# Optimization experiments

Hardware: AMD Instinct MI355X
Metric: run time of the kernel (lower is better)

The kernel has to match this reference:

```python
import jax, jax.numpy as jnp
import numpy as np

N = 100000   # nodes
E = 1600000  # edges
FEAT = 128
HID = 128
TGT = 64
L = 3
G = 512      # graphs in batch


def setup_inputs() -> dict:
    key = jax.random.key(0)
    ks = jax.random.split(key, 16)
    s = 0.05
    return {
        "x": jax.random.normal(ks[0], (N, FEAT), jnp.float32),
        "edge_index": jax.random.randint(ks[1], (2, E), 0, N, dtype=jnp.int32),
        "batch": jnp.sort(jax.random.randint(ks[2], (N,), 0, G, dtype=jnp.int32)),
        "conv_w1": jax.random.normal(ks[3], (L, FEAT, HID), jnp.float32) * s,
        "conv_b1": jax.random.normal(ks[4], (L, HID), jnp.float32) * s,
        "conv_w2": jax.random.normal(ks[5], (L, HID, HID), jnp.float32) * s,
        "conv_b2": jax.random.normal(ks[6], (L, HID), jnp.float32) * s,
        "eps": jnp.zeros((L,), jnp.float32),
        "gn_scale": jnp.ones((L, HID), jnp.float32),
        "gn_weight": jnp.ones((L, HID), jnp.float32),
        "gn_bias": jnp.zeros((L, HID), jnp.float32),
        "proj_w1": jax.random.normal(ks[7], (L, HID, HID), jnp.float32) * s,
        "proj_b1": jax.random.normal(ks[8], (L, HID), jnp.float32) * s,
        "proj_w2": jax.random.normal(ks[9], (L, HID, TGT), jnp.float32) * s,
        "proj_b2": jax.random.normal(ks[10], (L, TGT), jnp.float32) * s,
    }


def _graph_norm(h, batch, counts, scale, weight, bias):
    # per-graph mean -> scatter back to nodes
    mean = jax.ops.segment_sum(h, batch, num_segments=G) / counts
    sub = h - mean[batch] * scale
    var = jax.ops.segment_sum(sub * sub, batch, num_segments=G) / counts
    std = jnp.sqrt(var + 1e-8)
    return weight * sub / std[batch] + bias


def reference(x, edge_index, batch, conv_w1, conv_b1, conv_w2, conv_b2, eps,
              gn_scale, gn_weight, gn_bias, proj_w1, proj_b1, proj_w2, proj_b2):
    src, dst = edge_index[0], edge_index[1]
    counts = jnp.maximum(
        jax.ops.segment_sum(jnp.ones((N, 1), x.dtype), batch, num_segments=G), 1.0)
    h = x
    z_cat = []
    for l in range(L):
        # GINConv: aggr_j->i then 2-layer MLP
        aggr = jax.ops.segment_sum(h[src], dst, num_segments=N)
        h = (1.0 + eps[l]) * h + aggr
        h = jax.nn.relu(h @ conv_w1[l] + conv_b1[l]) @ conv_w2[l] + conv_b2[l]
        # GraphNorm
        h = _graph_norm(h, batch, counts, gn_scale[l], gn_weight[l], gn_bias[l])
        h = jax.nn.relu(h)
        # projection MLP + global add pool
        z = jax.nn.relu(h @ proj_w1[l] + proj_b1[l]) @ proj_w2[l] + proj_b2[l]
        z_cat.append(jax.ops.segment_sum(z, batch, num_segments=G))
    return jnp.concatenate(z_cat, axis=-1)  # [G, L*TGT]
```

## Files before the change

### kernel.cpp

```cpp
#include <hip/hip_runtime.h>

#define NN 100000
#define EE 1600000
#define HIDD 128
#define TGTT 64
#define GGG 512
#define NBK 98
#define CAPB 17408
#define ABLK 200
#define LSTR 136
#define CVTB 3125
#define GBLKG 1563
#define GBLKM 782
#define FOUTB 128
#define OUTB 128

typedef unsigned short ushort_t;
typedef __attribute__((ext_vector_type(8))) short short8;
typedef __attribute__((ext_vector_type(4))) float f32x4;
typedef __attribute__((ext_vector_type(4))) unsigned short us4;

__device__ __forceinline__ float b2f(ushort_t u) {
    union { unsigned int i; float f; } v; v.i = ((unsigned int)u) << 16; return v.f;
}
__device__ __forceinline__ ushort_t f2b(float f) {
    union { float f; unsigned int i; } v; v.f = f;
    unsigned int r = (v.i + 0x7fffu + ((v.i >> 16) & 1u)) >> 16;
    return (ushort_t)r;
}

__global__ __launch_bounds__(256) void k_pro(const float* __restrict__ x, ushort_t* __restrict__ Xb,
                                             const float* __restrict__ cw1, const float* __restrict__ cw2,
                                             const float* __restrict__ pw1, ushort_t* __restrict__ Wt,
                                             const int* __restrict__ batch, int* __restrict__ goff,
                                             const int* __restrict__ ei, int* __restrict__ gcnt,
                                             unsigned int* __restrict__ bbuf) {
    __shared__ ushort_t sW[128 * 129];
    __shared__ int cnt[NBK], base[NBK], cur[NBK];
    int b = blockIdx.x, t = threadIdx.x;

    if (b < CVTB) {
        long i0 = (long)b * 1024 + t;
#pragma unroll
        for (int c = 0; c < 4; c++) {
            long i = i0 + c * 256;
            float4 v = ((const float4*)x)[i];
            us4 o; o.x = f2b(v.x); o.y = f2b(v.y); o.z = f2b(v.z); o.w = f2b(v.w);
            ((us4*)Xb)[i] = o;
        }
        return;
    }
    b -= CVTB;
    if (b < 9) {
        int l = b / 3, j = b % 3;
        const float* src = (j == 0 ? cw1 : j == 1 ? cw2 : pw1) + (size_t)l * HIDD * HIDD;
        ushort_t* dst = Wt + (size_t)b * HIDD * HIDD;
        for (int i = t; i < HIDD * HIDD; i += 256) {
            int k = i >> 7, n = i & 127;
            sW[n * 129 + k] = f2b(src[i]);
        }
        __syncthreads();
        for (int i = t; i < HIDD * HIDD; i += 256) {
            dst[i] = sW[(i >> 7) * 129 + (i & 127)];
        }
        return;
    }
    b -= 9;
    if (b < 3) {
        int g = b * 256 + t;
        if (g > GGG) return;
        int lo = 0, hi = NN;
        while (lo < hi) { int mid = (lo + hi) >> 1; if (batch[mid] < g) lo = mid + 1; else hi = mid; }
        goff[g] = lo;
        return;
    }
    b -= 3;
    {
        if (t < NBK) cnt[t] = 0;
        __syncthreads();
        int e0 = b * 8000;
        int e1 = min(e0 + 8000, EE);
        for (int e = e0 + t; e < e1; e += 256)
            atomicAdd(&cnt[ei[EE + e] >> 10], 1);
        __syncthreads();
        if (t < NBK) { base[t] = atomicAdd(&gcnt[t], cnt[t]); cur[t] = 0; }
        __syncthreads();
        for (int e = e0 + t; e < e1; e += 256) {
            int s = ei[e], d = ei[EE + e];
            int bk = d >> 10;
            int off = base[bk] + atomicAdd(&cur[bk], 1);
            if (off < CAPB)
                bbuf[(long)bk * CAPB + off] = (unsigned int)s | (((unsigned int)d & 1023u) << 17);
        }
    }
}

__global__ __launch_bounds__(256) void k_csr(const int* __restrict__ gcnt,
                                             const unsigned int* __restrict__ bbuf,
                                             int* __restrict__ rowptr, int* __restrict__ csr) {
    __shared__ int ldeg[1024], lcur[1024], tsum[256], sb[NBK];
    int b = blockIdx.x, t = threadIdx.x;
    if (t < NBK) sb[t] = gcnt[t];
    __syncthreads();
    if (t == 0) { int a = 0; for (int i = 0; i < NBK; i++) { int v = sb[i]; sb[i] = a; a += v; } }
    __syncthreads();
    int cnt = min(gcnt[b], CAPB);
    int base = sb[b];
    const unsigned int* bb = bbuf + (long)b * CAPB;
#pragma unroll
    for (int i = 0; i < 4; i++) ldeg[t + 256 * i] = 0;
    __syncthreads();
    for (int i = t; i < cnt; i += 256) atomicAdd(&ldeg[bb[i] >> 17], 1);
    __syncthreads();
    int d0 = ldeg[4 * t], d1 = ldeg[4 * t + 1], d2 = ldeg[4 * t + 2], d3 = ldeg[4 * t + 3];
    int tot = d0 + d1 + d2 + d3;
    tsum[t] = tot;
    __syncthreads();
    for (int off = 1; off < 256; off <<= 1) {
        int u = (t >= off) ? tsum[t - off] : 0;
        __syncthreads();
        tsum[t] += u;
        __syncthreads();
    }
    int texcl = tsum[t] - tot;
    int p0 = base + texcl, p1 = p0 + d0, p2 = p1 + d1, p3 = p2 + d2;
    lcur[4 * t] = p0; lcur[4 * t + 1] = p1; lcur[4 * t + 2] = p2; lcur[4 * t + 3] = p3;
    int gnode = b * 1024 + 4 * t;
    if (gnode < NN)     rowptr[gnode]     = p0;
    if (gnode + 1 < NN) rowptr[gnode + 1] = p1;
    if (gnode + 2 < NN) rowptr[gnode + 2] = p2;
    if (gnode + 3 < NN) rowptr[gnode + 3] = p3;
    if (b == NBK - 1 && t == 0) rowptr[NN] = EE;
    __syncthreads();
    for (int i = t; i < cnt; i += 256) {
        unsigned int en = bb[i];
        int pos = atomicAdd(&lcur[en >> 17], 1);
        csr[pos] = (int)(en & 0x1FFFFu);
    }
}

__global__ __launch_bounds__(256, 8) void k_gather(const ushort_t* __restrict__ hin,
                                                   const int* __restrict__ rowptr,
                                                   const int* __restrict__ csr,
                                                   const float* __restrict__ eps, int l,
                                                   ushort_t* __restrict__ aggr,
                                                   const float* __restrict__ pooledP, const int* __restrict__ goff,
                                                   const float* __restrict__ WoP, const float* __restrict__ BoP,
                                                   float* __restrict__ outP, int lprev) {
    int tid = threadIdx.x;

    if (blockIdx.x >= GBLKG) {
        if (lprev < 0) return;
        int ob = blockIdx.x - GBLKG;
        int sub = tid >> 6, tt = tid & 63;
        int g = ob * 4 + sub;
        if (g >= GGG) return;
        float cntg = (float)(goff[g + 1] - goff[g]);
        float acc = cntg * BoP[tt];
        const float* p = pooledP + (long)g * HIDD;
        for (int k = 0; k < HIDD; k++) acc += p[k] * WoP[k * TGTT + tt];
        outP[(long)g * (3 * TGTT) + lprev * TGTT + tt] = acc;
        return;
    }

    long base = (long)blockIdx.x * 64;
    int lane = tid & 15, ng = tid >> 4;
    int off = lane << 3;
    float e1 = 1.0f + eps[l];

#pragma unroll 1
    for (int it = 0; it < 4; it++) {
        int row = it * 16 + ng;
        long node = base + row;
        if (node < NN) {
            short8 h = *(const short8*)(hin + (node << 7) + off);
            float acc[8];
#pragma unroll
            for (int t = 0; t < 8; t++) acc[t] = e1 * b2f((ushort_t)h[t]);
            int jb = rowptr[node], je = rowptr[node + 1];
            int j = jb;
            for (; j + 8 <= je; j += 8) {
                int s0 = csr[j], s1 = csr[j + 1], s2 = csr[j + 2], s3 = csr[j + 3];
                int s4 = csr[j + 4], s5 = csr[j + 5], s6 = csr[j + 6], s7 = csr[j + 7];
                short8 v0 = *(const short8*)(hin + ((long)s0 << 7) + off);
                short8 v1 = *(const short8*)(hin + ((long)s1 << 7) + off);
                short8 v2 = *(const short8*)(hin + ((long)s2 << 7) + off);
                short8 v3 = *(const short8*)(hin + ((long)s3 << 7) + off);
                short8 v4 = *(const short8*)(hin + ((long)s4 << 7) + off);
                short8 v5 = *(const short8*)(hin + ((long)s5 << 7) + off);
                short8 v6 = *(const short8*)(hin + ((long)s6 << 7) + off);
                short8 v7 = *(const short8*)(hin + ((long)s7 << 7) + off);
#pragma unroll
                for (int t = 0; t < 8; t++)
                    acc[t] += ((b2f((ushort_t)v0[t]) + b2f((ushort_t)v1[t])) +
                               (b2f((ushort_t)v2[t]) + b2f((ushort_t)v3[t]))) +
                              ((b2f((ushort_t)v4[t]) + b2f((ushort_t)v5[t])) +
                               (b2f((ushort_t)v6[t]) + b2f((ushort_t)v7[t])));
            }
            for (; j + 4 <= je; j += 4) {
                int s0 = csr[j], s1 = csr[j + 1], s2 = csr[j + 2], s3 = csr[j + 3];
                short8 v0 = *(const short8*)(hin + ((long)s0 << 7) + off);
                short8 v1 = *(const short8*)(hin + ((long)s1 << 7) + off);
                short8 v2 = *(const short8*)(hin + ((long)s2 << 7) + off);
                short8 v3 = *(const short8*)(hin + ((long)s3 << 7) + off);
#pragma unroll
                for (int t = 0; t < 8; t++)
                    acc[t] += (b2f((ushort_t)v0[t]) + b2f((ushort_t)v1[t])) +
                              (b2f((ushort_t)v2[t]) + b2f((ushort_t)v3[t]));
            }
            for (; j < je; j++) {
                int s = csr[j];
                short8 v = *(const short8*)(hin + ((long)s << 7) + off);
#pragma unroll
                for (int t = 0; t < 8; t++) acc[t] += b2f((ushort_t)v[t]);
            }
            short8 o;
#pragma unroll
            for (int t = 0; t < 8; t++) o[t] = (short)f2b(acc[t]);
            *(short8*)(aggr + (node << 7) + off) = o;
        }
    }
}

__global__ __launch_bounds__(256) void k_mlp(const ushort_t* __restrict__ aggr,
                                             const ushort_t* __restrict__ Wt1, const float* __restrict__ B1,
                                             const ushort_t* __restrict__ Wt2, const float* __restrict__ B2,
                                             ushort_t* __restrict__ Y) {
    __shared__ ushort_t sX[128 * LSTR];
    int tid = threadIdx.x;
    long base = (long)blockIdx.x * 128;

#pragma unroll
    for (int c = 0; c < 8; c++) {
        int idx = c * 256 + tid;
        int row = idx >> 4, cw = idx & 15;
        long grow = base + row;
        short8 v = (short8)0;
        if (grow < NN) v = *(const short8*)(aggr + (grow << 7) + (cw << 3));
        *(short8*)(sX + row * LSTR + (cw << 3)) = v;
    }
    __syncthreads();

    int w = tid >> 6, l64 = tid & 63, q = l64 >> 4, l16 = l64 & 15;
    int r0 = w * 16, r1 = 64 + w * 16;
    short8 a0[4], a1[4];
#pragma unroll
    for (int c = 0; c < 4; c++) {
        a0[c] = *(const short8*)(sX + (r0 + l16) * LSTR + q * 8 + c * 32);
        a1[c] = *(const short8*)(sX + (r1 + l16) * LSTR + q * 8 + c * 32);
    }
    f32x4 acc0[8], acc1[8];
#pragma unroll
    for (int nt = 0; nt < 8; nt++) {
        int col = nt * 16 + l16;
        float bias = B1[col];
        f32x4 c0 = {bias, bias, bias, bias};
        f32x4 c1 = c0;
        const ushort_t* bB = Wt1 + col * HIDD + q * 8;
#pragma unroll
        for (int c = 0; c < 4; c++) {
            short8 b = *(const short8*)(bB + c * 32);
            c0 = __builtin_amdgcn_mfma_f32_16x16x32_bf16(a0[c], b, c0, 0, 0, 0);
            c1 = __builtin_amdgcn_mfma_f32_16x16x32_bf16(a1[c], b, c1, 0, 0, 0);
        }
        acc0[nt] = c0; acc1[nt] = c1;
    }
#pragma unroll
    for (int nt = 0; nt < 8; nt++) {
        int col = nt * 16 + l16;
#pragma unroll
        for (int r = 0; r < 4; r++) {
            sX[(r0 + q * 4 + r) * LSTR + col] = f2b(fmaxf(acc0[nt][r], 0.f));
            sX[(r1 + q * 4 + r) * LSTR + col] = f2b(fmaxf(acc1[nt][r], 0.f));
        }
    }
#pragma unroll
    for (int c = 0; c < 4; c++) {
        a0[c] = *(const short8*)(sX + (r0 + l16) * LSTR + q * 8 + c * 32);
        a1[c] = *(const short8*)(sX + (r1 + l16) * LSTR + q * 8 + c * 32);
    }
#pragma unroll
    for (int nt = 0; nt < 8; nt++) {
        int col = nt * 16 + l16;
        float bias = B2[col];
        f32x4 c0 = {bias, bias, bias, bias};
        f32x4 c1 = c0;
        const ushort_t* bB = Wt2 + col * HIDD + q * 8;
#pragma unroll
        for (int c = 0; c < 4; c++) {
            short8 b = *(const short8*)(bB + c * 32);
            c0 = __builtin_amdgcn_mfma_f32_16x16x32_bf16(a0[c], b, c0, 0, 0, 0);
            c1 = __builtin_amdgcn_mfma_f32_16x16x32_bf16(a1[c], b, c1, 0, 0, 0);
        }
#pragma unroll
        for (int r = 0; r < 4; r++) {
            long row0 = base + r0 + q * 4 + r;
            long row1 = base + r1 + q * 4 + r;
            if (row0 < NN) Y[(row0 << 7) + col] = f2b(c0[r]);
            if (row1 < NN) Y[(row1 << 7) + col] = f2b(c1[r]);
        }
    }
}

__global__ __launch_bounds__(512) void k_gstat(const ushort_t* __restrict__ Hraw,
                                               const int* __restrict__ goff,
                                               const float* __restrict__ scale,
                                               const float* __restrict__ weight,
                                               float* __restrict__ msb, float* __restrict__ invb,
                                               float* __restrict__ pooled) {
    __shared__ float red[2][32][128];
    int g = blockIdx.x;
    int s = goff[g], e = goff[g + 1];
    float cnt = (float)max(e - s, 1);
    int lane = threadIdx.x & 15;
    int rg = threadIdx.x >> 4;
    int f0 = lane << 3;
    float sum[8], sq[8];
#pragma unroll
    for (int t = 0; t < 8; t++) { sum[t] = 0.f; sq[t] = 0.f; }
    for (int i = s + rg; i < e; i += 32) {
        short8 v = *(const short8*)(Hraw + ((long)i << 7) + f0);
#pragma unroll
        for (int t = 0; t < 8; t++) { float a = b2f((ushort_t)v[t]); sum[t] += a; sq[t] += a * a; }
    }
#pragma unroll
    for (int t = 0; t < 8; t++) { red[0][rg][f0 + t] = sum[t]; red[1][rg][f0 + t] = sq[t]; }
    __syncthreads();
    for (int off = 16; off > 0; off >>= 1) {
        if (rg < off) {
#pragma unroll
            for (int t = 0; t < 8; t++) {
                red[0][rg][f0 + t] += red[0][rg + off][f0 + t];
                red[1][rg][f0 + t] += red[1][rg + off][f0 + t];
            }
        }
        __syncthreads();
    }
    if (rg == 0) {
#pragma unroll
        for (int t = 0; t < 8; t++) {
            int f = f0 + t;
            float mean = red[0][0][f] / cnt;
            float ms = mean * scale[f];
            float var = red[1][0][f] / cnt - 2.f * ms * mean + ms * ms;
            msb[g * HIDD + f] = ms;
            invb[g * HIDD + f] = weight[f] / sqrtf(var + 1e-8f);
            pooled[g * HIDD + f] = 0.f;
        }
    }
}

__global__ __launch_bounds__(256) void k_projpool(const ushort_t* __restrict__ Hraw,
                                                  const int* __restrict__ batch,
                                                  const float* __restrict__ msb, const float* __restrict__ invb,
                                                  const float* __restrict__ gnb,
                                                  const ushort_t* __restrict__ Wt, const float* __restrict__ B,
                                                  ushort_t* __restrict__ Hn, float* __restrict__ pooled,
                                                  int store_hn) {
    __shared__ ushort_t sX[128 * LSTR];
    __shared__ int sgid[128];
    int tid = threadIdx.x;
    long base = (long)blockIdx.x * 128;
#pragma unroll
    for (int c = 0; c < 8; c++) {
        int idx = c * 256 + tid;
        int row = idx >> 4, cw = idx & 15;
        long grow = base + row;
        short8 v = (short8)0;
        if (grow < NN) {
            short8 raw = *(const short8*)(Hraw + (grow << 7) + (cw << 3));
            int g = batch[grow];
            if (cw == 0) sgid[row] = g;
            const float* msp = msb + g * HIDD + (cw << 3);
            const float* ivp = invb + g * HIDD + (cw << 3);
            const float* gbp = gnb + (cw << 3);
            float4 m0 = *(const float4*)msp, m1 = *(const float4*)(msp + 4);
            float4 i0 = *(const float4*)ivp, i1 = *(const float4*)(ivp + 4);
            float4 g0 = *(const float4*)gbp, g1 = *(const float4*)(gbp + 4);
            float mv[8] = {m0.x, m0.y, m0.z, m0.w, m1.x, m1.y, m1.z, m1.w};
            float iv[8] = {i0.x, i0.y, i0.z, i0.w, i1.x, i1.y, i1.z, i1.w};
            float gv[8] = {g0.x, g0.y, g0.z, g0.w, g1.x, g1.y, g1.z, g1.w};
#pragma unroll
            for (int t = 0; t < 8; t++) {
                float val = (b2f((ushort_t)raw[t]) - mv[t]) * iv[t] + gv[t];
                v[t] = (short)f2b(val > 0.f ? val : 0.f);
            }
            if (store_hn) *(short8*)(Hn + (grow << 7) + (cw << 3)) = v;
        } else if (cw == 0) {
            sgid[row] = -1;
        }
        *(short8*)(sX + row * LSTR + (cw << 3)) = v;
    }
    __syncthreads();

    int w = tid >> 6, l64 = tid & 63, q = l64 >> 4, l16 = l64 & 15;
    int r0 = w * 16, r1 = 64 + w * 16;
    short8 a0[4], a1[4];
#pragma unroll
    for (int c = 0; c < 4; c++) {
        a0[c] = *(const short8*)(sX + (r0 + l16) * LSTR + q * 8 + c * 32);
        a1[c] = *(const short8*)(sX + (r1 + l16) * LSTR + q * 8 + c * 32);
    }
    f32x4 acc0[8], acc1[8];
#pragma unroll
    for (int nt = 0; nt < 8; nt++) {
        int col = nt * 16 + l16;
        float bias = B[col];
        f32x4 c0 = {bias, bias, bias, bias};
        f32x4 c1 = c0;
        const ushort_t* bB = Wt + col * HIDD + q * 8;
#pragma unroll
        for (int c = 0; c < 4; c++) {
            short8 b = *(const short8*)(bB + c * 32);
            c0 = __builtin_amdgcn_mfma_f32_16x16x32_bf16(a0[c], b, c0, 0, 0, 0);
            c1 = __builtin_amdgcn_mfma_f32_16x16x32_bf16(a1[c], b, c1, 0, 0, 0);
        }
        acc0[nt] = c0; acc1[nt] = c1;
    }
#pragma unroll
    for (int nt = 0; nt < 8; nt++) {
        int col = nt * 16 + l16;
#pragma unroll
        for (int r = 0; r < 4; r++) {
            sX[(r0 + q * 4 + r) * LSTR + col] = f2b(fmaxf(acc0[nt][r], 0.f));
            sX[(r1 + q * 4 + r) * LSTR + col] = f2b(fmaxf(acc1[nt][r], 0.f));
        }
    }
    __syncthreads();

    int f = tid & 127, half = tid >> 7;
    int rbeg = half * 64, rend = rbeg + 64;
    float sum = 0.f;
    int curg = -1;
    for (int row = rbeg; row < rend; row++) {
        int g = sgid[row];
        if (g != curg) {
            if (curg >= 0) atomicAdd(&pooled[(long)curg * HIDD + f], sum);
            sum = 0.f; curg = g;
        }
        if (g >= 0) sum += b2f(sX[row * LSTR + f]);
    }
    if (curg >= 0) atomicAdd(&pooled[(long)curg * HIDD + f], sum);
}

__global__ __launch_bounds__(256) void k_out(const float* __restrict__ pooled, const int* __restrict__ goff,
                                             const float* __restrict__ W, const float* __restrict__ B,
                                             float* __restrict__ out, int l) {
    int sub = threadIdx.x >> 6, tt = threadIdx.x & 63;
    int g = blockIdx.x * 4 + sub;
    if (g >= GGG) return;
    float cnt = (float)(goff[g + 1] - goff[g]);
    float acc = cnt * B[tt];
    const float* p = pooled + (long)g * HIDD;
    for (int k = 0; k < HIDD; k++) acc += p[k] * W[k * TGTT + tt];
    out[(long)g * (3 * TGTT) + l * TGTT + tt] = acc;
}

extern "C" void kernel_launch(void* const* d_in, const int* in_sizes, int n_in,
                              void* d_out, int out_size, void* d_ws, size_t ws_size,
                              hipStream_t stream) {
    const float* x    = (const float*)d_in[0];
    const int*   ei   = (const int*)d_in[1];
    const int*   batch= (const int*)d_in[2];
    const float* cw1  = (const float*)d_in[3];
    const float* cb1  = (const float*)d_in[4];
    const float* cw2  = (const float*)d_in[5];
    const float* cb2  = (const float*)d_in[6];
    const float* eps  = (const float*)d_in[7];
    const float* gsc  = (const float*)d_in[8];
    const float* gw   = (const float*)d_in[9];
    const float* gb   = (const float*)d_in[10];
    const float* pw1  = (const float*)d_in[11];
    const float* pb1  = (const float*)d_in[12];
    const float* pw2  = (const float*)d_in[13];
    const float* pb2  = (const float*)d_in[14];
    float* out = (float*)d_out;

    ushort_t* Xb   = (ushort_t*)d_ws;
    ushort_t* Hn   = Xb;
    ushort_t* Hraw = Xb + (size_t)NN * HIDD;
    ushort_t* Wt   = Hraw + (size_t)NN * HIDD;
    float* msb     = (float*)(Wt + (size_t)9 * HIDD * HIDD);
    float* invb    = msb + (size_t)GGG * HIDD;
    float* pooled  = invb + (size_t)GGG * HIDD;
    int* goff   = (int*)(pooled + (size_t)GGG * HIDD);
    int* rowptr = goff + (GGG + 1);
    int* gcnt   = rowptr + (NN + 1);
    int* csr    = gcnt + NBK;
    unsigned int* bbuf = (unsigned int*)(csr + EE);

    hipMemsetAsync(gcnt, 0, NBK * sizeof(int), stream);
    k_pro<<<CVTB + 9 + 3 + ABLK, 256, 0, stream>>>(x, Xb, cw1, cw2, pw1, Wt, batch, goff, ei, gcnt, bbuf);
    k_csr<<<NBK, 256, 0, stream>>>(gcnt, bbuf, rowptr, csr);

    for (int l = 0; l < 3; l++) {
        const ushort_t* hin = (l == 0) ? Xb : Hn;
        ushort_t* Wt1 = Wt + (size_t)(l * 3 + 0) * HIDD * HIDD;
        ushort_t* Wt2 = Wt + (size_t)(l * 3 + 1) * HIDD * HIDD;
        ushort_t* Wtp = Wt + (size_t)(l * 3 + 2) * HIDD * HIDD;
        int grid = GBLKG + (l > 0 ? FOUTB : 0);
        k_gather<<<grid, 256, 0, stream>>>(hin, rowptr, csr, eps, l, Hraw,
                                           pooled, goff,
                                           pw2 + (size_t)(l - 1) * HIDD * TGTT, pb2 + (l - 1) * TGTT,
                                           out, l - 1);
        k_mlp<<<GBLKM, 256, 0, stream>>>(Hraw, Wt1, cb1 + l * HIDD, Wt2, cb2 + l * HIDD, Hraw);
        k_gstat<<<GGG, 512, 0, stream>>>(Hraw, goff, gsc + l * HIDD, gw + l * HIDD, msb, invb, pooled);
        k_projpool<<<GBLKM, 256, 0, stream>>>(Hraw, batch, msb, invb, gb + l * HIDD,
                                              Wtp, pb1 + l * HIDD, Hn, pooled, (l < 2) ? 1 : 0);
    }
    k_out<<<OUTB, 256, 0, stream>>>(pooled, goff, pw2 + (size_t)2 * HIDD * TGTT, pb2 + 2 * TGTT, out, 2);
}
```

Baseline: 632.8 us.

## Fuse GraphNorm statistics into MLP epilogue and widen CSR build kernels

Per-graph sum and sum-of-squares are now accumulated inside the MLP kernel from the shared-memory tile of outputs, using segmented runs and global atomics. This replaces the separate k_gstat pass that re-read the whole hidden matrix, and a tiny k_gfin kernel finishes the statistics and zeroes the accumulators. The edge bucketing uses four times as many blocks, k_csr runs with 1024 threads and one node per thread, and the weight transpose drops its shared-memory staging. Float atomics make the reduction order nondeterministic, and gsum/gsq reuse the bbuf scratch region after the CSR build.

```diff
diff --git a/kernel.cpp b/kernel.cpp
--- a/kernel.cpp
+++ b/kernel.cpp
@@ -7,7 +7,8 @@
 #define GGG 512
 #define NBK 98
 #define CAPB 17408
-#define ABLK 200
+#define ABLK 800
+#define EPB 2000
 #define LSTR 136
 #define CVTB 3125
 #define GBLKG 1563
@@ -35,7 +36,6 @@
                                              const int* __restrict__ batch, int* __restrict__ goff,
                                              const int* __restrict__ ei, int* __restrict__ gcnt,
                                              unsigned int* __restrict__ bbuf) {
-    __shared__ ushort_t sW[128 * 129];
     __shared__ int cnt[NBK], base[NBK], cur[NBK];
     int b = blockIdx.x, t = threadIdx.x;
 
@@ -55,14 +55,8 @@
         int l = b / 3, j = b % 3;
         const float* src = (j == 0 ? cw1 : j == 1 ? cw2 : pw1) + (size_t)l * HIDD * HIDD;
         ushort_t* dst = Wt + (size_t)b * HIDD * HIDD;
-        for (int i = t; i < HIDD * HIDD; i += 256) {
-            int k = i >> 7, n = i & 127;
-            sW[n * 129 + k] = f2b(src[i]);
-        }
-        __syncthreads();
-        for (int i = t; i < HIDD * HIDD; i += 256) {
-            dst[i] = sW[(i >> 7) * 129 + (i & 127)];
-        }
+        for (int i = t; i < HIDD * HIDD; i += 256)
+            dst[i] = f2b(src[(i & 127) * HIDD + (i >> 7)]);
         return;
     }
     b -= 9;
@@ -78,8 +72,8 @@
     {
         if (t < NBK) cnt[t] = 0;
         __syncthreads();
-        int e0 = b * 8000;
-        int e1 = min(e0 + 8000, EE);
+        int e0 = b * EPB;
+        int e1 = min(e0 + EPB, EE);
         for (int e = e0 + t; e < e1; e += 256)
             atomicAdd(&cnt[ei[EE + e] >> 10], 1);
         __syncthreads();
@@ -95,46 +89,39 @@
     }
 }
 
-__global__ __launch_bounds__(256) void k_csr(const int* __restrict__ gcnt,
-                                             const unsigned int* __restrict__ bbuf,
-                                             int* __restrict__ rowptr, int* __restrict__ csr) {
-    __shared__ int ldeg[1024], lcur[1024], tsum[256], sb[NBK];
+__global__ __launch_bounds__(1024) void k_csr(const int* __restrict__ gcnt,
+                                              const unsigned int* __restrict__ bbuf,
+                                              int* __restrict__ rowptr, int* __restrict__ csr) {
+    __shared__ int ldeg[1024], tsum[1024], sb[NBK];
     int b = blockIdx.x, t = threadIdx.x;
     if (t < NBK) sb[t] = gcnt[t];
+    ldeg[t] = 0;
     __syncthreads();
     if (t == 0) { int a = 0; for (int i = 0; i < NBK; i++) { int v = sb[i]; sb[i] = a; a += v; } }
     __syncthreads();
     int cnt = min(gcnt[b], CAPB);
     int base = sb[b];
     const unsigned int* bb = bbuf + (long)b * CAPB;
-#pragma unroll
-    for (int i = 0; i < 4; i++) ldeg[t + 256 * i] = 0;
-    __syncthreads();
-    for (int i = t; i < cnt; i += 256) atomicAdd(&ldeg[bb[i] >> 17], 1);
-    __syncthreads();
-    int d0 = ldeg[4 * t], d1 = ldeg[4 * t + 1], d2 = ldeg[4 * t + 2], d3 = ldeg[4 * t + 3];
-    int tot = d0 + d1 + d2 + d3;
-    tsum[t] = tot;
-    __syncthreads();
-    for (int off = 1; off < 256; off <<= 1) {
+    for (int i = t; i < cnt; i += 1024) atomicAdd(&ldeg[bb[i] >> 17], 1);
+    __syncthreads();
+    int d0 = ldeg[t];
+    tsum[t] = d0;
+    __syncthreads();
+    for (int off = 1; off < 1024; off <<= 1) {
         int u = (t >= off) ? tsum[t - off] : 0;
         __syncthreads();
         tsum[t] += u;
         __syncthreads();
     }
-    int texcl = tsum[t] - tot;
-    int p0 = base + texcl, p1 = p0 + d0, p2 = p1 + d1, p3 = p2 + d2;
-    lcur[4 * t] = p0; lcur[4 * t + 1] = p1; lcur[4 * t + 2] = p2; lcur[4 * t + 3] = p3;
-    int gnode = b * 1024 + 4 * t;
-    if (gnode < NN)     rowptr[gnode]     = p0;
-    if (gnode + 1 < NN) rowptr[gnode + 1] = p1;
-    if (gnode + 2 < NN) rowptr[gnode + 2] = p2;
-    if (gnode + 3 < NN) rowptr[gnode + 3] = p3;
+    int p0 = base + tsum[t] - d0;
+    int gnode = b * 1024 + t;
+    if (gnode < NN) rowptr[gnode] = p0;
     if (b == NBK - 1 && t == 0) rowptr[NN] = EE;
-    __syncthreads();
-    for (int i = t; i < cnt; i += 256) {
+    ldeg[t] = p0;
+    __syncthreads();
+    for (int i = t; i < cnt; i += 1024) {
         unsigned int en = bb[i];
-        int pos = atomicAdd(&lcur[en >> 17], 1);
+        int pos = atomicAdd(&ldeg[en >> 17], 1);
         csr[pos] = (int)(en & 0x1FFFFu);
     }
 }
@@ -223,10 +210,13 @@
 }
 
 __global__ __launch_bounds__(256) void k_mlp(const ushort_t* __restrict__ aggr,
+                                             const int* __restrict__ batch,
                                              const ushort_t* __restrict__ Wt1, const float* __restrict__ B1,
                                              const ushort_t* __restrict__ Wt2, const float* __restrict__ B2,
-                                             ushort_t* __restrict__ Y) {
+                                             ushort_t* __restrict__ Y,
+                                             float* __restrict__ gsum, float* __restrict__ gsq) {
     __shared__ ushort_t sX[128 * LSTR];
+    __shared__ int sgid[128];
     int tid = threadIdx.x;
     long base = (long)blockIdx.x * 128;
 
@@ -236,7 +226,12 @@
         int row = idx >> 4, cw = idx & 15;
         long grow = base + row;
         short8 v = (short8)0;
-        if (grow < NN) v = *(const short8*)(aggr + (grow << 7) + (cw << 3));
+        if (grow < NN) {
+            v = *(const short8*)(aggr + (grow << 7) + (cw << 3));
+            if (cw == 0) sgid[row] = batch[grow];
+        } else if (cw == 0) {
+            sgid[row] = -1;
+        }
         *(short8*)(sX + row * LSTR + (cw << 3)) = v;
     }
     __syncthreads();
@@ -296,58 +291,52 @@
         for (int r = 0; r < 4; r++) {
             long row0 = base + r0 + q * 4 + r;
             long row1 = base + r1 + q * 4 + r;
-            if (row0 < NN) Y[(row0 << 7) + col] = f2b(c0[r]);
-            if (row1 < NN) Y[(row1 << 7) + col] = f2b(c1[r]);
-        }
-    }
-}
-
-__global__ __launch_bounds__(512) void k_gstat(const ushort_t* __restrict__ Hraw,
-                                               const int* __restrict__ goff,
-                                               const float* __restrict__ scale,
-                                               const float* __restrict__ weight,
-                                               float* __restrict__ msb, float* __restrict__ invb,
-                                               float* __restrict__ pooled) {
-    __shared__ float red[2][32][128];
-    int g = blockIdx.x;
-    int s = goff[g], e = goff[g + 1];
-    float cnt = (float)max(e - s, 1);
-    int lane = threadIdx.x & 15;
-    int rg = threadIdx.x >> 4;
-    int f0 = lane << 3;
-    float sum[8], sq[8];
-#pragma unroll
-    for (int t = 0; t < 8; t++) { sum[t] = 0.f; sq[t] = 0.f; }
-    for (int i = s + rg; i < e; i += 32) {
-        short8 v = *(const short8*)(Hraw + ((long)i << 7) + f0);
-#pragma unroll
-        for (int t = 0; t < 8; t++) { float a = b2f((ushort_t)v[t]); sum[t] += a; sq[t] += a * a; }
-    }
-#pragma unroll
-    for (int t = 0; t < 8; t++) { red[0][rg][f0 + t] = sum[t]; red[1][rg][f0 + t] = sq[t]; }
-    __syncthreads();
-    for (int off = 16; off > 0; off >>= 1) {
-        if (rg < off) {
-#pragma unroll
-            for (int t = 0; t < 8; t++) {
-                red[0][rg][f0 + t] += red[0][rg + off][f0 + t];
-                red[1][rg][f0 + t] += red[1][rg + off][f0 + t];
+            ushort_t h0 = f2b(c0[r]), h1 = f2b(c1[r]);
+            if (row0 < NN) Y[(row0 << 7) + col] = h0;
+            if (row1 < NN) Y[(row1 << 7) + col] = h1;
+            sX[(r0 + q * 4 + r) * LSTR + col] = h0;
+            sX[(r1 + q * 4 + r) * LSTR + col] = h1;
+        }
+    }
+    __syncthreads();
+
+    int f = tid & 127, half = tid >> 7;
+    int rbeg = half * 64, rend = rbeg + 64;
+    float s1 = 0.f, s2 = 0.f;
+    int curg = -1;
+    for (int row = rbeg; row < rend; row++) {
+        int g = sgid[row];
+        if (g != curg) {
+            if (curg >= 0) {
+                atomicAdd(&gsum[(long)curg * HIDD + f], s1);
+                atomicAdd(&gsq[(long)curg * HIDD + f], s2);
             }
-        }
-        __syncthreads();
-    }
-    if (rg == 0) {
-#pragma unroll
-        for (int t = 0; t < 8; t++) {
-            int f = f0 + t;
-            float mean = red[0][0][f] / cnt;
-            float ms = mean * scale[f];
-            float var = red[1][0][f] / cnt - 2.f * ms * mean + ms * ms;
-            msb[g * HIDD + f] = ms;
-            invb[g * HIDD + f] = weight[f] / sqrtf(var + 1e-8f);
-            pooled[g * HIDD + f] = 0.f;
-        }
-    }
+            s1 = 0.f; s2 = 0.f; curg = g;
+        }
+        if (g >= 0) { float a = b2f(sX[row * LSTR + f]); s1 += a; s2 += a * a; }
+    }
+    if (curg >= 0) {
+        atomicAdd(&gsum[(long)curg * HIDD + f], s1);
+        atomicAdd(&gsq[(long)curg * HIDD + f], s2);
+    }
+}
+
+__global__ __launch_bounds__(128) void k_gfin(float* __restrict__ gsum, float* __restrict__ gsq,
+                                              const int* __restrict__ goff,
+                                              const float* __restrict__ scale, const float* __restrict__ weight,
+                                              float* __restrict__ msb, float* __restrict__ invb,
+                                              float* __restrict__ pooled) {
+    int g = blockIdx.x, f = threadIdx.x;
+    float cnt = (float)max(goff[g + 1] - goff[g], 1);
+    long i = (long)g * HIDD + f;
+    float mean = gsum[i] / cnt;
+    float ms = mean * scale[f];
+    float var = gsq[i] / cnt - 2.f * ms * mean + ms * ms;
+    msb[i] = ms;
+    invb[i] = weight[f] / sqrtf(var + 1e-8f);
+    pooled[i] = 0.f;
+    gsum[i] = 0.f;
+    gsq[i] = 0.f;
 }
 
 __global__ __launch_bounds__(256) void k_projpool(const ushort_t* __restrict__ Hraw,
@@ -488,10 +477,13 @@
     int* gcnt   = rowptr + (NN + 1);
     int* csr    = gcnt + NBK;
     unsigned int* bbuf = (unsigned int*)(csr + EE);
+    float* gsum = (float*)bbuf;
+    float* gsq  = gsum + (size_t)GGG * HIDD;
 
     hipMemsetAsync(gcnt, 0, NBK * sizeof(int), stream);
     k_pro<<<CVTB + 9 + 3 + ABLK, 256, 0, stream>>>(x, Xb, cw1, cw2, pw1, Wt, batch, goff, ei, gcnt, bbuf);
-    k_csr<<<NBK, 256, 0, stream>>>(gcnt, bbuf, rowptr, csr);
+    k_csr<<<NBK, 1024, 0, stream>>>(gcnt, bbuf, rowptr, csr);
+    hipMemsetAsync(gsum, 0, (size_t)2 * GGG * HIDD * sizeof(float), stream);
 
     for (int l = 0; l < 3; l++) {
         const ushort_t* hin = (l == 0) ? Xb : Hn;
@@ -503,8 +495,9 @@
                                            pooled, goff,
                                            pw2 + (size_t)(l - 1) * HIDD * TGTT, pb2 + (l - 1) * TGTT,
                                            out, l - 1);
-        k_mlp<<<GBLKM, 256, 0, stream>>>(Hraw, Wt1, cb1 + l * HIDD, Wt2, cb2 + l * HIDD, Hraw);
-        k_gstat<<<GGG, 512, 0, stream>>>(Hraw, goff, gsc + l * HIDD, gw + l * HIDD, msb, invb, pooled);
+        k_mlp<<<GBLKM, 256, 0, stream>>>(Hraw, batch, Wt1, cb1 + l * HIDD, Wt2, cb2 + l * HIDD, Hraw,
+                                         gsum, gsq);
+        k_gfin<<<GGG, 128, 0, stream>>>(gsum, gsq, goff, gsc + l * HIDD, gw + l * HIDD, msb, invb, pooled);
         k_projpool<<<GBLKM, 256, 0, stream>>>(Hraw, batch, msb, invb, gb + l * HIDD,
                                               Wtp, pb1 + l * HIDD, Hn, pooled, (l < 2) ? 1 : 0);
     }
```

After: 651.4 us. 1.03x slower.
